# Kernel tuning notes

Measured on AMD Instinct MI355X. Metric: run time of the kernel, lower is better.

Reference implementation:

```python
import jax, jax.numpy as jnp
import numpy as np

BETA = 1.0

def setup_inputs() -> dict:
    key = jax.random.key(0)
    kX, ks = jax.random.split(key)
    P, N = 8192, 1024
    X = jax.random.normal(kX, (P, N), dtype=jnp.float32)
    s = jax.random.normal(ks, (P - 1, N), dtype=jnp.float32)
    return {"X": X, "s": s}

def reference(X, s):
    # score = softmax(beta * s @ X[:-1]^T, axis=1)  -> (P-1, P-1)
    score = jax.nn.softmax(BETA * jnp.einsum('qn,pn->qp', s, X[:-1]), axis=1)
    # output = score @ X[1:]  -> (P-1, N)
    return jnp.einsum('qp,pn->qn', score, X[1:])
```

## Files before the change

### kernel.cpp

```cpp
#include <hip/hip_runtime.h>
#include <math.h>


#define NQ 8191
#define NK 8191
#define DD 1024
#define BQ 64
#define BK 256
#define KSPLIT 2
#define KHALF 4096
#define ITERS 16
#define NW 8
#define NT 512
#define QKK 31

typedef _Float16 half8 __attribute__((ext_vector_type(8)));
typedef float float4v __attribute__((ext_vector_type(4)));

__global__ void prep_kf(const float* __restrict__ X, _Float16* __restrict__ Kf) {
    int b = blockIdx.x * 256 + threadIdx.x;
    int l  = b & 63;
    int kk = (b >> 6) & 31;
    int g  = b >> 11;
    int row = g * 16 + (l & 15);
    int col = kk * 32 + ((l >> 4) << 3);
    const float4v* src = (const float4v*)&X[(size_t)row * DD + col];
    float4v v0 = src[0], v1 = src[1];
    half8 h;
    h[0]=(_Float16)v0[0]; h[1]=(_Float16)v0[1]; h[2]=(_Float16)v0[2]; h[3]=(_Float16)v0[3];
    h[4]=(_Float16)v1[0]; h[5]=(_Float16)v1[1]; h[6]=(_Float16)v1[2]; h[7]=(_Float16)v1[3];
    *(half8*)&Kf[(size_t)b * 8] = h;
}

__global__ void prep_vf(const float* __restrict__ X, _Float16* __restrict__ Vf) {
    int b = blockIdx.x * 256 + threadIdx.x;
    int l   = b & 63;
    int kkg = (b >> 6) & 255;
    int h   = b >> 14;
    int d    = h * 16 + (l & 15);
    int key0 = kkg * 32 + ((l >> 4) << 3);
    half8 hv;
    #pragma unroll
    for (int e = 0; e < 8; ++e) {
        int row = key0 + e + 1;
        float v = (row < 8192) ? X[(size_t)row * DD + d] : 0.f;
        hv[e] = (_Float16)v;
    }
    *(half8*)&Vf[(size_t)b * 8] = hv;
}

__launch_bounds__(NT, 2)
__global__ void flash(const float* __restrict__ s,
                      const _Float16* __restrict__ Kf,
                      const _Float16* __restrict__ Vf,
                      _Float16* __restrict__ Op,
                      float2* __restrict__ ml) {
    __shared__ _Float16 Qf[4 * QKK * 64 * 8];
    __shared__ _Float16 Pf[4 * 8 * 64 * 8];
    __shared__ float    Rm[NW * BQ];

    const int t  = threadIdx.x;
    const int w  = t >> 6;
    const int l  = t & 63;
    const int ln = l & 15;
    const int q4 = l >> 4;
    const int qt = blockIdx.x >> 1;
    const int ks = blockIdx.x & 1;
    const int q0 = qt * BQ;

    for (int e = t; e < 4 * QKK * 64; e += NT) {
        int ll  = e & 63;
        int rem = e >> 6;
        int kk  = rem % QKK;
        int qf  = rem / QKK;
        int row = qf * 16 + (ll & 15);
        int col = kk * 32 + ((ll >> 4) << 3);
        half8 hv;
        if (q0 + row < NQ) {
            const float4v* src = (const float4v*)&s[(size_t)(q0 + row) * DD + col];
            float4v v0 = src[0], v1 = src[1];
            hv[0]=(_Float16)v0[0]; hv[1]=(_Float16)v0[1]; hv[2]=(_Float16)v0[2]; hv[3]=(_Float16)v0[3];
            hv[4]=(_Float16)v1[0]; hv[5]=(_Float16)v1[1]; hv[6]=(_Float16)v1[2]; hv[7]=(_Float16)v1[3];
        } else {
            #pragma unroll
            for (int j = 0; j < 8; ++j) hv[j] = (_Float16)0.f;
        }
        *(half8*)&Qf[(size_t)e * 8] = hv;
    }
    half8 qreg[4];
    #pragma unroll
    for (int qf = 0; qf < 4; ++qf) {
        int row = qf * 16 + ln;
        int col = QKK * 32 + (q4 << 3);
        half8 hv;
        if (q0 + row < NQ) {
            const float4v* src = (const float4v*)&s[(size_t)(q0 + row) * DD + col];
            float4v v0 = src[0], v1 = src[1];
            hv[0]=(_Float16)v0[0]; hv[1]=(_Float16)v0[1]; hv[2]=(_Float16)v0[2]; hv[3]=(_Float16)v0[3];
            hv[4]=(_Float16)v1[0]; hv[5]=(_Float16)v1[1]; hv[6]=(_Float16)v1[2]; hv[7]=(_Float16)v1[3];
        } else {
            #pragma unroll
            for (int j = 0; j < 8; ++j) hv[j] = (_Float16)0.f;
        }
        qreg[qf] = hv;
    }
    __syncthreads();

    float4v o[4][8];
    #pragma unroll
    for (int qf = 0; qf < 4; ++qf)
        #pragma unroll
        for (int dt = 0; dt < 8; ++dt)
            o[qf][dt] = (float4v){0.f, 0.f, 0.f, 0.f};

    float m_run[16], l_run[16];
    #pragma unroll
    for (int i = 0; i < 16; ++i) { m_run[i] = -INFINITY; l_run[i] = 0.f; }

    const int pbase = w * 512 + q4 * 32 + ((ln >> 3) << 7) + (ln & 7);

    for (int it = 0; it < ITERS; ++it) {
        const _Float16* kp0 = Kf + (size_t)(ks * 256 + it * 16 + w * 2) * 16384 + (size_t)l * 8;
        float4v sa[4][2];
        #pragma unroll
        for (int qf = 0; qf < 4; ++qf) {
            sa[qf][0] = (float4v){0.f, 0.f, 0.f, 0.f};
            sa[qf][1] = (float4v){0.f, 0.f, 0.f, 0.f};
        }
        #pragma unroll 4
        for (int kk = 0; kk < QKK; ++kk) {
            half8 k0 = *(const half8*)(kp0 + kk * 512);
            half8 k1 = *(const half8*)(kp0 + 16384 + kk * 512);
            #pragma unroll
            for (int qf = 0; qf < 4; ++qf) {
                half8 qa = *(const half8*)&Qf[((qf * QKK + kk) * 64 + l) * 8];
                sa[qf][0] = __builtin_amdgcn_mfma_f32_16x16x32_f16(qa, k0, sa[qf][0], 0, 0, 0);
                sa[qf][1] = __builtin_amdgcn_mfma_f32_16x16x32_f16(qa, k1, sa[qf][1], 0, 0, 0);
            }
        }
        {
            half8 k0 = *(const half8*)(kp0 + 31 * 512);
            half8 k1 = *(const half8*)(kp0 + 16384 + 31 * 512);
            #pragma unroll
            for (int qf = 0; qf < 4; ++qf) {
                sa[qf][0] = __builtin_amdgcn_mfma_f32_16x16x32_f16(qreg[qf], k0, sa[qf][0], 0, 0, 0);
                sa[qf][1] = __builtin_amdgcn_mfma_f32_16x16x32_f16(qreg[qf], k1, sa[qf][1], 0, 0, 0);
            }
        }

        const int kbase = ks * KHALF + it * BK + w * 32;
        const bool bad0 = (kbase + ln) >= NK;
        const bool bad1 = (kbase + 16 + ln) >= NK;

        float pm[16];
        #pragma unroll
        for (int qf = 0; qf < 4; ++qf)
            #pragma unroll
            for (int r = 0; r < 4; ++r) {
                float v0 = bad0 ? -INFINITY : sa[qf][0][r];
                float v1 = bad1 ? -INFINITY : sa[qf][1][r];
                pm[qf * 4 + r] = fmaxf(v0, v1);
            }
        #pragma unroll
        for (int i = 0; i < 16; ++i) {
            float v = pm[i];
            v = fmaxf(v, __shfl_xor(v, 1, 64));
            v = fmaxf(v, __shfl_xor(v, 2, 64));
            v = fmaxf(v, __shfl_xor(v, 4, 64));
            v = fmaxf(v, __shfl_xor(v, 8, 64));
            pm[i] = v;
        }
        if (ln == 0) {
            #pragma unroll
            for (int qf = 0; qf < 4; ++qf)
                #pragma unroll
                for (int r = 0; r < 4; ++r)
                    Rm[w * BQ + qf * 16 + q4 * 4 + r] = pm[qf * 4 + r];
        }
        __syncthreads();

        float al[16];
        #pragma unroll
        for (int qf = 0; qf < 4; ++qf)
            #pragma unroll
            for (int r = 0; r < 4; ++r) {
                int row = qf * 16 + q4 * 4 + r;
                int i = qf * 4 + r;
                float v = m_run[i];
                #pragma unroll
                for (int wv = 0; wv < NW; ++wv) v = fmaxf(v, Rm[wv * BQ + row]);
                al[i] = __expf(m_run[i] - v);
                m_run[i] = v;
            }
        #pragma unroll
        for (int i = 0; i < 16; ++i) l_run[i] *= al[i];
        #pragma unroll
        for (int qf = 0; qf < 4; ++qf)
            #pragma unroll
            for (int r = 0; r < 4; ++r) {
                int i = qf * 4 + r;
                float p0 = bad0 ? 0.f : __expf(sa[qf][0][r] - m_run[i]);
                float p1 = bad1 ? 0.f : __expf(sa[qf][1][r] - m_run[i]);
                l_run[i] += p0 + p1;
                Pf[pbase + qf * 4096 + r * 8]       = (_Float16)p0;
                Pf[pbase + qf * 4096 + r * 8 + 256] = (_Float16)p1;
            }
        #pragma unroll
        for (int qf = 0; qf < 4; ++qf)
            #pragma unroll
            for (int dt = 0; dt < 8; ++dt)
                #pragma unroll
                for (int r = 0; r < 4; ++r)
                    o[qf][dt][r] *= al[qf * 4 + r];
        __syncthreads();

        const _Float16* vp = Vf + (size_t)(w * 8) * 131072
                             + (size_t)(ks * 128 + it * 8) * 512 + (size_t)l * 8;
        #pragma unroll 2
        for (int kk2 = 0; kk2 < 8; ++kk2) {
            half8 pa[4];
            #pragma unroll
            for (int qf = 0; qf < 4; ++qf)
                pa[qf] = *(const half8*)&Pf[((qf * 8 + kk2) * 64 + l) * 8];
            #pragma unroll
            for (int dt = 0; dt < 8; ++dt) {
                half8 vf = *(const half8*)(vp + (size_t)dt * 131072 + kk2 * 512);
                #pragma unroll
                for (int qf = 0; qf < 4; ++qf)
                    o[qf][dt] = __builtin_amdgcn_mfma_f32_16x16x32_f16(pa[qf], vf, o[qf][dt], 0, 0, 0);
            }
        }
        __syncthreads();
    }

    float lt[16];
    #pragma unroll
    for (int i = 0; i < 16; ++i) {
        float v = l_run[i];
        v += __shfl_xor(v, 1, 64);
        v += __shfl_xor(v, 2, 64);
        v += __shfl_xor(v, 4, 64);
        v += __shfl_xor(v, 8, 64);
        lt[i] = v;
    }
    if (ln == 0) {
        #pragma unroll
        for (int qf = 0; qf < 4; ++qf)
            #pragma unroll
            for (int r = 0; r < 4; ++r)
                Rm[w * BQ + qf * 16 + q4 * 4 + r] = lt[qf * 4 + r];
    }
    __syncthreads();

    float lsum[16], inv[16];
    #pragma unroll
    for (int qf = 0; qf < 4; ++qf)
        #pragma unroll
        for (int r = 0; r < 4; ++r) {
            int row = qf * 16 + q4 * 4 + r;
            float sum = 0.f;
            #pragma unroll
            for (int wv = 0; wv < NW; ++wv) sum += Rm[wv * BQ + row];
            lsum[qf * 4 + r] = sum;
            inv[qf * 4 + r] = 1.f / sum;
        }

    if (w == 0 && ln == 0) {
        #pragma unroll
        for (int qf = 0; qf < 4; ++qf)
            #pragma unroll
            for (int r = 0; r < 4; ++r) {
                int row = q0 + qf * 16 + q4 * 4 + r;
                int i = qf * 4 + r;
                if (row < NQ)
                    ml[ks * 8192 + row] = make_float2(m_run[i], lsum[i]);
            }
    }

    #pragma unroll
    for (int qf = 0; qf < 4; ++qf)
        #pragma unroll
        for (int dt = 0; dt < 8; ++dt)
            #pragma unroll
            for (int r = 0; r < 4; ++r) {
                int row = q0 + qf * 16 + q4 * 4 + r;
                int col = w * 128 + dt * 16 + ln;
                if (row < NQ)
                    Op[((size_t)ks * NQ + row) * DD + col] =
                        (_Float16)(o[qf][dt][r] * inv[qf * 4 + r]);
            }
}

__global__ void combine(const _Float16* __restrict__ Op,
                        const float2* __restrict__ ml,
                        float* __restrict__ out) {
    size_t idx = ((size_t)blockIdx.x * 256 + threadIdx.x) * 8;
    if (idx >= (size_t)NQ * DD) return;
    int row = (int)(idx >> 10);
    float2 a = ml[row];
    float2 b = ml[8192 + row];
    float m  = fmaxf(a.x, b.x);
    float w0 = a.y * __expf(a.x - m);
    float w1 = b.y * __expf(b.x - m);
    float inv = 1.f / (w0 + w1);
    w0 *= inv; w1 *= inv;
    half8 h0 = *(const half8*)&Op[idx];
    half8 h1 = *(const half8*)&Op[(size_t)NQ * DD + idx];
    float4v o0, o1;
    #pragma unroll
    for (int e = 0; e < 4; ++e) o0[e] = w0 * (float)h0[e] + w1 * (float)h1[e];
    #pragma unroll
    for (int e = 0; e < 4; ++e) o1[e] = w0 * (float)h0[e + 4] + w1 * (float)h1[e + 4];
    *(float4v*)&out[idx]     = o0;
    *(float4v*)&out[idx + 4] = o1;
}

extern "C" void kernel_launch(void* const* d_in, const int* in_sizes, int n_in,
                              void* d_out, int out_size, void* d_ws, size_t ws_size,
                              hipStream_t stream) {
    const float* X = (const float*)d_in[0];
    const float* s = (const float*)d_in[1];
    float* out = (float*)d_out;

    _Float16* Kf = (_Float16*)d_ws;
    _Float16* Vf = Kf + (size_t)8192 * 1024;
    _Float16* Op = Vf + (size_t)8192 * 1024;
    float2*   ml = (float2*)(Op + (size_t)2 * NQ * DD);

    prep_kf<<<4096, 256, 0, stream>>>(X, Kf);
    prep_vf<<<4096, 256, 0, stream>>>(X, Vf);
    flash<<<KSPLIT * ((NQ + BQ - 1) / BQ), NT, 0, stream>>>(s, Kf, Vf, Op, ml);
    combine<<<4096, 256, 0, stream>>>(Op, ml, out);
}
```

Measured before the change: 683.8 us.

## Stage V tiles through LDS with async global_load_lds triple buffering, shrink Q LDS

The PV loop now streams V fragments into three per-wave LDS buffers using global_load_lds, with explicit vmcnt waits, so global V loads overlap the MFMAs. To free LDS for these buffers, the resident Q tile shrinks from 31 to 19 k-chunks, and the remaining 13 chunks are read from a new pre-converted fp16 Q buffer in global memory, produced by an extra prep kernel. This trades more global/L2 traffic for Q and an extra launch against better latency hiding on V, and relies on hand-placed wait counts being correct.

Result: slower. 744.2 us (+8.8%).

```diff
diff --git a/kernel.cpp b/kernel.cpp
--- a/kernel.cpp
+++ b/kernel.cpp
@@ -12,7 +12,7 @@
 #define ITERS 16
 #define NW 8
 #define NT 512
-#define QKK 31
+#define QKK 19
 
 typedef _Float16 half8 __attribute__((ext_vector_type(8)));
 typedef float float4v __attribute__((ext_vector_type(4)));
@@ -49,8 +49,69 @@
     *(half8*)&Vf[(size_t)b * 8] = hv;
 }
 
+__global__ void prep_qf(const float* __restrict__ s, _Float16* __restrict__ Qg) {
+    int b = blockIdx.x * 256 + threadIdx.x;
+    int l  = b & 63;
+    int kk = (b >> 6) & 31;
+    int qf = (b >> 11) & 3;
+    int qt = b >> 13;
+    int row = qt * 64 + qf * 16 + (l & 15);
+    int col = kk * 32 + ((l >> 4) << 3);
+    half8 hv;
+    if (row < NQ) {
+        const float4v* src = (const float4v*)&s[(size_t)row * DD + col];
+        float4v v0 = src[0], v1 = src[1];
+        hv[0]=(_Float16)v0[0]; hv[1]=(_Float16)v0[1]; hv[2]=(_Float16)v0[2]; hv[3]=(_Float16)v0[3];
+        hv[4]=(_Float16)v1[0]; hv[5]=(_Float16)v1[1]; hv[6]=(_Float16)v1[2]; hv[7]=(_Float16)v1[3];
+    } else {
+        #pragma unroll
+        for (int j = 0; j < 8; ++j) hv[j] = (_Float16)0.f;
+    }
+    *(half8*)&Qg[(size_t)b * 8] = hv;
+}
+
+__device__ __forceinline__ void gld16(const _Float16* g, _Float16* lp) {
+    __builtin_amdgcn_global_load_lds(
+        (const __attribute__((address_space(1))) unsigned int*)g,
+        (__attribute__((address_space(3))) unsigned int*)lp, 16, 0, 0);
+}
+
+#define W4 do { asm volatile("s_waitcnt vmcnt(4)" ::: "memory"); \
+                __builtin_amdgcn_sched_barrier(0); } while (0)
+#define W2 do { asm volatile("s_waitcnt vmcnt(2)" ::: "memory"); \
+                __builtin_amdgcn_sched_barrier(0); } while (0)
+#define W0 do { asm volatile("s_waitcnt vmcnt(0)" ::: "memory"); \
+                __builtin_amdgcn_sched_barrier(0); } while (0)
+#define NOWAIT ((void)0)
+#define NOFILL ((void)0)
+
+#define IVF(ARR, DT0, KK2N) do { \
+    gld16(vbase + (((size_t)(w * 8 + (DT0)    ) * 256 + (KK2N)) << 9), &ARR[w][0][0]); \
+    gld16(vbase + (((size_t)(w * 8 + (DT0) + 1) * 256 + (KK2N)) << 9), &ARR[w][1][0]); \
+} while (0)
+
+#define PV3(S, ARR, WAITM, FILLC) do { \
+    WAITM; \
+    if (((S) & 3) == 0) { \
+        _Pragma("unroll") \
+        for (int qf_ = 0; qf_ < 4; ++qf_) \
+            pa[qf_] = *(const half8*)&Pf[((qf_ * 8 + ((S) >> 2)) * 64 + l) * 8]; \
+    } \
+    { \
+        half8 v0_ = *(const half8*)&ARR[w][0][l * 8]; \
+        half8 v1_ = *(const half8*)&ARR[w][1][l * 8]; \
+        _Pragma("unroll") \
+        for (int qf_ = 0; qf_ < 4; ++qf_) { \
+            o[qf_][((S) & 3) * 2]     = __builtin_amdgcn_mfma_f32_16x16x32_f16(pa[qf_], v0_, o[qf_][((S) & 3) * 2], 0, 0, 0); \
+            o[qf_][((S) & 3) * 2 + 1] = __builtin_amdgcn_mfma_f32_16x16x32_f16(pa[qf_], v1_, o[qf_][((S) & 3) * 2 + 1], 0, 0, 0); \
+        } \
+    } \
+    FILLC; \
+} while (0)
+
 __launch_bounds__(NT, 2)
 __global__ void flash(const float* __restrict__ s,
+                      const _Float16* __restrict__ Qg,
                       const _Float16* __restrict__ Kf,
                       const _Float16* __restrict__ Vf,
                       _Float16* __restrict__ Op,
@@ -58,15 +119,20 @@
     __shared__ _Float16 Qf[4 * QKK * 64 * 8];
     __shared__ _Float16 Pf[4 * 8 * 64 * 8];
     __shared__ float    Rm[NW * BQ];
+    __shared__ _Float16 VSA[NW][2][512];
+    __shared__ _Float16 VSB[NW][2][512];
+    __shared__ _Float16 VSC[NW][2][512];
 
     const int t  = threadIdx.x;
     const int w  = t >> 6;
     const int l  = t & 63;
     const int ln = l & 15;
     const int q4 = l >> 4;
-    const int qt = blockIdx.x >> 1;
-    const int ks = blockIdx.x & 1;
-    const int q0 = qt * BQ;
+
+    const int bid = blockIdx.x;
+    const int qt  = bid >> 1;
+    const int ks  = bid & 1;
+    const int q0  = qt * BQ;
 
     for (int e = t; e < 4 * QKK * 64; e += NT) {
         int ll  = e & 63;
@@ -87,23 +153,6 @@
         }
         *(half8*)&Qf[(size_t)e * 8] = hv;
     }
-    half8 qreg[4];
-    #pragma unroll
-    for (int qf = 0; qf < 4; ++qf) {
-        int row = qf * 16 + ln;
-        int col = QKK * 32 + (q4 << 3);
-        half8 hv;
-        if (q0 + row < NQ) {
-            const float4v* src = (const float4v*)&s[(size_t)(q0 + row) * DD + col];
-            float4v v0 = src[0], v1 = src[1];
-            hv[0]=(_Float16)v0[0]; hv[1]=(_Float16)v0[1]; hv[2]=(_Float16)v0[2]; hv[3]=(_Float16)v0[3];
-            hv[4]=(_Float16)v1[0]; hv[5]=(_Float16)v1[1]; hv[6]=(_Float16)v1[2]; hv[7]=(_Float16)v1[3];
-        } else {
-            #pragma unroll
-            for (int j = 0; j < 8; ++j) hv[j] = (_Float16)0.f;
-        }
-        qreg[qf] = hv;
-    }
     __syncthreads();
 
     float4v o[4][8];
@@ -118,6 +167,7 @@
     for (int i = 0; i < 16; ++i) { m_run[i] = -INFINITY; l_run[i] = 0.f; }
 
     const int pbase = w * 512 + q4 * 32 + ((ln >> 3) << 7) + (ln & 7);
+    half8 pa[4];
 
     for (int it = 0; it < ITERS; ++it) {
         const _Float16* kp0 = Kf + (size_t)(ks * 256 + it * 16 + w * 2) * 16384 + (size_t)l * 8;
@@ -138,13 +188,15 @@
                 sa[qf][1] = __builtin_amdgcn_mfma_f32_16x16x32_f16(qa, k1, sa[qf][1], 0, 0, 0);
             }
         }
-        {
-            half8 k0 = *(const half8*)(kp0 + 31 * 512);
-            half8 k1 = *(const half8*)(kp0 + 16384 + 31 * 512);
+        #pragma unroll 4
+        for (int kk = QKK; kk < 32; ++kk) {
+            half8 k0 = *(const half8*)(kp0 + kk * 512);
+            half8 k1 = *(const half8*)(kp0 + 16384 + kk * 512);
             #pragma unroll
             for (int qf = 0; qf < 4; ++qf) {
-                sa[qf][0] = __builtin_amdgcn_mfma_f32_16x16x32_f16(qreg[qf], k0, sa[qf][0], 0, 0, 0);
-                sa[qf][1] = __builtin_amdgcn_mfma_f32_16x16x32_f16(qreg[qf], k1, sa[qf][1], 0, 0, 0);
+                half8 qa = *(const half8*)(Qg + (((size_t)(qt * 4 + qf) * 32 + kk) << 9) + (l << 3));
+                sa[qf][0] = __builtin_amdgcn_mfma_f32_16x16x32_f16(qa, k0, sa[qf][0], 0, 0, 0);
+                sa[qf][1] = __builtin_amdgcn_mfma_f32_16x16x32_f16(qa, k1, sa[qf][1], 0, 0, 0);
             }
         }
 
@@ -179,6 +231,7 @@
         }
         __syncthreads();
 
+        const _Float16* vbase = Vf + (((size_t)(ks * 128 + it * 8)) << 9) + (l << 3);
         float al[16];
         #pragma unroll
         for (int qf = 0; qf < 4; ++qf)
@@ -192,6 +245,11 @@
                 al[i] = __expf(m_run[i] - v);
                 m_run[i] = v;
             }
+
+        IVF(VSA, 0, 0);
+        IVF(VSB, 2, 0);
+        IVF(VSC, 4, 0);
+
         #pragma unroll
         for (int i = 0; i < 16; ++i) l_run[i] *= al[i];
         #pragma unroll
@@ -214,22 +272,38 @@
                     o[qf][dt][r] *= al[qf * 4 + r];
         __syncthreads();
 
-        const _Float16* vp = Vf + (size_t)(w * 8) * 131072
-                             + (size_t)(ks * 128 + it * 8) * 512 + (size_t)l * 8;
-        #pragma unroll 2
-        for (int kk2 = 0; kk2 < 8; ++kk2) {
-            half8 pa[4];
-            #pragma unroll
-            for (int qf = 0; qf < 4; ++qf)
-                pa[qf] = *(const half8*)&Pf[((qf * 8 + kk2) * 64 + l) * 8];
-            #pragma unroll
-            for (int dt = 0; dt < 8; ++dt) {
-                half8 vf = *(const half8*)(vp + (size_t)dt * 131072 + kk2 * 512);
-                #pragma unroll
-                for (int qf = 0; qf < 4; ++qf)
-                    o[qf][dt] = __builtin_amdgcn_mfma_f32_16x16x32_f16(pa[qf], vf, o[qf][dt], 0, 0, 0);
-            }
-        }
+        PV3(0,  VSA, NOWAIT, IVF(VSA, 6, 0));
+        PV3(1,  VSB, NOWAIT, IVF(VSB, 0, 1));
+        PV3(2,  VSC, NOWAIT, IVF(VSC, 2, 1));
+        PV3(3,  VSA, W4,     IVF(VSA, 4, 1));
+        PV3(4,  VSB, W4,     IVF(VSB, 6, 1));
+        PV3(5,  VSC, W4,     IVF(VSC, 0, 2));
+        PV3(6,  VSA, W4,     IVF(VSA, 2, 2));
+        PV3(7,  VSB, W4,     IVF(VSB, 4, 2));
+        PV3(8,  VSC, W4,     IVF(VSC, 6, 2));
+        PV3(9,  VSA, W4,     IVF(VSA, 0, 3));
+        PV3(10, VSB, W4,     IVF(VSB, 2, 3));
+        PV3(11, VSC, W4,     IVF(VSC, 4, 3));
+        PV3(12, VSA, W4,     IVF(VSA, 6, 3));
+        PV3(13, VSB, W4,     IVF(VSB, 0, 4));
+        PV3(14, VSC, W4,     IVF(VSC, 2, 4));
+        PV3(15, VSA, W4,     IVF(VSA, 4, 4));
+        PV3(16, VSB, W4,     IVF(VSB, 6, 4));
+        PV3(17, VSC, W4,     IVF(VSC, 0, 5));
+        PV3(18, VSA, W4,     IVF(VSA, 2, 5));
+        PV3(19, VSB, W4,     IVF(VSB, 4, 5));
+        PV3(20, VSC, W4,     IVF(VSC, 6, 5));
+        PV3(21, VSA, W4,     IVF(VSA, 0, 6));
+        PV3(22, VSB, W4,     IVF(VSB, 2, 6));
+        PV3(23, VSC, W4,     IVF(VSC, 4, 6));
+        PV3(24, VSA, W4,     IVF(VSA, 6, 6));
+        PV3(25, VSB, W4,     IVF(VSB, 0, 7));
+        PV3(26, VSC, W4,     IVF(VSC, 2, 7));
+        PV3(27, VSA, W4,     IVF(VSA, 4, 7));
+        PV3(28, VSB, W4,     IVF(VSB, 6, 7));
+        PV3(29, VSC, W4,     NOFILL);
+        PV3(30, VSA, W2,     NOFILL);
+        PV3(31, VSB, W0,     NOFILL);
         __syncthreads();
     }
 
@@ -324,11 +398,13 @@
 
     _Float16* Kf = (_Float16*)d_ws;
     _Float16* Vf = Kf + (size_t)8192 * 1024;
-    _Float16* Op = Vf + (size_t)8192 * 1024;
+    _Float16* Qg = Vf + (size_t)8192 * 1024;
+    _Float16* Op = Qg + (size_t)8192 * 1024;
     float2*   ml = (float2*)(Op + (size_t)2 * NQ * DD);
 
     prep_kf<<<4096, 256, 0, stream>>>(X, Kf);
     prep_vf<<<4096, 256, 0, stream>>>(X, Vf);
-    flash<<<KSPLIT * ((NQ + BQ - 1) / BQ), NT, 0, stream>>>(s, Kf, Vf, Op, ml);
+    prep_qf<<<4096, 256, 0, stream>>>(s, Qg);
+    flash<<<KSPLIT * ((NQ + BQ - 1) / BQ), NT, 0, stream>>>(s, Qg, Kf, Vf, Op, ml);
     combine<<<4096, 256, 0, stream>>>(Op, ml, out);
 }
```
